# Kernel optimization log

Hardware: AMD Instinct MI355X
Metric: run time of the kernel (lower is better)

Reference implementation:

```python
import jax, jax.numpy as jnp
import numpy as np

B, S, T, D, ST, C = 128, 37, 2048, 256, 8, 2  # batch, sensors, time, d_model, static, classes
MERGED = D + ST


def setup_inputs() -> dict:
    key = jax.random.key(0)
    ks = jax.random.split(key, 14)
    u = lambda k, shape, fan: jax.random.uniform(k, shape, jnp.float32, -1.0, 1.0) / np.sqrt(fan)
    return {
        "x": jax.random.normal(ks[0], (B, S, T), jnp.float32),
        "static": jax.random.normal(ks[1], (B, ST), jnp.float32),
        "time": jax.random.uniform(ks[2], (B, T), jnp.float32),
        "sensor_mask": jax.random.randint(ks[3], (B, S, T), 0, 2).astype(jnp.int32),
        # learned params (torch Linear stored here as [in, out])
        "W_sensor": u(ks[4], (2 * S, D), 2 * S),
        "b_sensor": u(ks[5], (D,), 2 * S),
        "W_time": u(ks[6], (1, D), 1),
        "b_time": u(ks[7], (D,), 1),
        "W_static": u(ks[8], (ST, ST), ST),
        "b_static": u(ks[9], (ST,), ST),
        "W_merge": u(ks[10], (MERGED, MERGED), MERGED),
        "b_merge": u(ks[11], (MERGED,), MERGED),
        "W_cls": u(ks[12], (MERGED, C), MERGED),
        "b_cls": u(ks[13], (C,), MERGED),
    }


def reference(x, static, time, sensor_mask, W_sensor, b_sensor, W_time, b_time,
              W_static, b_static, W_merge, b_merge, W_cls, b_cls):
    # [B,S,T] -> [B,T,S]; concat measurements with (float) sensor mask -> [B,T,2S]
    x_t = jnp.transpose(x, (0, 2, 1))
    m_t = jnp.transpose(sensor_mask, (0, 2, 1)).astype(jnp.float32)
    x_time = jnp.concatenate([x_t, m_t], axis=2)
    # timestep valid-mask: any nonzero feature at that step
    mask = (jnp.sum(x_time != 0, axis=2) > 0).astype(jnp.float32)  # [B,T]
    # sensor embedding + time encoding
    h = jnp.einsum('btf,fd->btd', x_time, W_sensor) + b_sensor
    h = h + time[..., None] * W_time[0] + b_time  # Linear(1, D) on time
    # NOTE: Mamba2ForCausalLM(vocab_size=0) produces logits with size(-1)==0,
    # so the original forward falls back to last_hidden_states = x_time (= h).
    # masked mean pooling over time
    denom = jnp.clip(jnp.sum(mask, axis=1), 1e-9)[:, None]  # [B,1]
    pooled = jnp.sum(h * mask[..., None], axis=1) / denom  # [B,D]
    static_e = static @ W_static + b_static  # [B,ST]
    comb = jnp.concatenate([pooled, static_e], axis=1)  # [B,MERGED]
    comb = jax.nn.relu(comb @ W_merge + b_merge)
    return comb @ W_cls + b_cls  # [B,C]
```

## Files before the change

### kernel.cpp

```cpp
#include <hip/hip_runtime.h>
#include <hip/hip_bf16.h>

#define BB   128
#define SS   37
#define TT   2048
#define DD   256
#define STT  8
#define CC   2
#define MER  264
#define FF   74

#define NC    8
#define CHUNK (TT / NC)
#define RW    76
#define NSW   10

__global__ __launch_bounds__(256) void reduce_kernel(
    const float* __restrict__ x,
    const int*   __restrict__ smk,
    const float* __restrict__ tarr,
    float* __restrict__ red)
{
    const int blk   = blockIdx.x;
    const int b     = blk >> 3;
    const int chunk = blk & 7;
    const int t0    = chunk * CHUNK;
    const int wave  = threadIdx.x >> 6;
    const int lane  = threadIdx.x & 63;

    float ax[NSW];
    float am[NSW];
    unsigned nz = 0;

#pragma unroll
    for (int si = 0; si < NSW; ++si) {
        const int s = wave + 4 * si;
        if (s < SS) {
            const size_t base = ((size_t)(b * SS + s)) * TT + t0 + 4 * lane;
            const float4 xv = *(const float4*)(x + base);
            const int4   mv = *(const int4*)(smk + base);
            ax[si] = (xv.x + xv.y) + (xv.z + xv.w);
            am[si] = (float)((mv.x + mv.y) + (mv.z + mv.w));
            nz |= ((xv.x != 0.f) | (mv.x != 0)) ? 1u : 0u;
            nz |= ((xv.y != 0.f) | (mv.y != 0)) ? 2u : 0u;
            nz |= ((xv.z != 0.f) | (mv.z != 0)) ? 4u : 0u;
            nz |= ((xv.w != 0.f) | (mv.w != 0)) ? 8u : 0u;
        } else {
            ax[si] = 0.f; am[si] = 0.f;
        }
    }

    __shared__ unsigned nzp[4][64];
    nzp[wave][lane] = nz;
    __syncthreads();

    if (wave == 0) {
        const unsigned m = nzp[0][lane] | nzp[1][lane] | nzp[2][lane] | nzp[3][lane];
        const float4 tv = *(const float4*)(tarr + (size_t)b * TT + t0 + 4 * lane);
        float cnt = 0.f, tsum = 0.f;
        if (m & 1u) { cnt += 1.f; tsum += tv.x; }
        if (m & 2u) { cnt += 1.f; tsum += tv.y; }
        if (m & 4u) { cnt += 1.f; tsum += tv.z; }
        if (m & 8u) { cnt += 1.f; tsum += tv.w; }
        for (int off = 32; off; off >>= 1) {
            cnt  += __shfl_down(cnt,  off, 64);
            tsum += __shfl_down(tsum, off, 64);
        }
        if (lane == 0) {
            atomicAdd(&red[b * RW + 74], cnt);
            atomicAdd(&red[b * RW + 75], tsum);
        }
    }

#pragma unroll
    for (int si = 0; si < NSW; ++si) {
        const int s = wave + 4 * si;
        if (s < SS) {
            float vx = ax[si], vm = am[si];
            for (int off = 32; off; off >>= 1) {
                vx += __shfl_down(vx, off, 64);
                vm += __shfl_down(vm, off, 64);
            }
            if (lane == 0) {
                atomicAdd(&red[b * RW + s],      vx);
                atomicAdd(&red[b * RW + SS + s], vm);
            }
        }
    }
}

__global__ __launch_bounds__(320) void head_kernel(
    const float* __restrict__ red,
    const float* __restrict__ statics,
    const float* __restrict__ W_sensor,
    const float* __restrict__ b_sensor,
    const float* __restrict__ W_time,
    const float* __restrict__ b_time,
    const float* __restrict__ W_static,
    const float* __restrict__ b_static,
    const float* __restrict__ W_merge,
    const float* __restrict__ b_merge,
    const float* __restrict__ W_cls,
    const float* __restrict__ b_cls,
    float* __restrict__ out)
{
    const int b   = blockIdx.x;
    const int tid = threadIdx.x;

    __shared__ float sred[RW];
    __shared__ float comb[MER];
    __shared__ float comb2[MER];
    __shared__ float rbuf[10];

    if (tid < RW) sred[tid] = red[b * RW + tid];
    __syncthreads();

    const float smask = sred[74];
    const float stime = sred[75];
    const float inv   = 1.0f / fmaxf(smask, 1e-9f);

    if (tid < DD) {
        const int d = tid;
        float a0 = smask * (b_sensor[d] + b_time[d]) + stime * W_time[d];
        float a1 = 0.f;
#pragma unroll
        for (int f = 0; f < FF; f += 2) {
            a0 += sred[f]     * W_sensor[f * DD + d];
            a1 += sred[f + 1] * W_sensor[(f + 1) * DD + d];
        }
        comb[d] = (a0 + a1) * inv;
    } else if (tid < DD + STT) {
        const int j = tid - DD;
        float acc = b_static[j];
#pragma unroll
        for (int i = 0; i < STT; ++i)
            acc += statics[b * STT + i] * W_static[i * STT + j];
        comb[DD + j] = acc;
    }
    __syncthreads();

    if (tid < MER) {
        const int j = tid;
        float a[8];
#pragma unroll
        for (int k = 0; k < 8; ++k) a[k] = 0.f;
        for (int i = 0; i < MER; i += 8) {
#pragma unroll
            for (int k = 0; k < 8; ++k)
                a[k] += comb[i + k] * W_merge[(i + k) * MER + j];
        }
        const float acc = b_merge[j] +
            ((a[0] + a[1]) + (a[2] + a[3])) + ((a[4] + a[5]) + (a[6] + a[7]));
        comb2[j] = fmaxf(acc, 0.f);
    }
    __syncthreads();

    float c0 = 0.f, c1 = 0.f;
    if (tid < MER) {
        const float v = comb2[tid];
        c0 = v * W_cls[tid * CC];
        c1 = v * W_cls[tid * CC + 1];
    }
    for (int off = 32; off; off >>= 1) {
        c0 += __shfl_down(c0, off, 64);
        c1 += __shfl_down(c1, off, 64);
    }
    const int wv = tid >> 6, ln = tid & 63;
    if (ln == 0) { rbuf[wv] = c0; rbuf[5 + wv] = c1; }
    __syncthreads();
    if (tid == 0)
        out[b * CC + 0] = b_cls[0] + rbuf[0] + rbuf[1] + rbuf[2] + rbuf[3] + rbuf[4];
    if (tid == 1)
        out[b * CC + 1] = b_cls[1] + rbuf[5] + rbuf[6] + rbuf[7] + rbuf[8] + rbuf[9];
}

extern "C" void kernel_launch(void* const* d_in, const int* in_sizes, int n_in,
                              void* d_out, int out_size, void* d_ws, size_t ws_size,
                              hipStream_t stream) {
    const float* x        = (const float*)d_in[0];
    const float* statics  = (const float*)d_in[1];
    const float* tarr     = (const float*)d_in[2];
    const int*   smk      = (const int*)  d_in[3];
    const float* W_sensor = (const float*)d_in[4];
    const float* b_sensor = (const float*)d_in[5];
    const float* W_time   = (const float*)d_in[6];
    const float* b_time   = (const float*)d_in[7];
    const float* W_static = (const float*)d_in[8];
    const float* b_static = (const float*)d_in[9];
    const float* W_merge  = (const float*)d_in[10];
    const float* b_merge  = (const float*)d_in[11];
    const float* W_cls    = (const float*)d_in[12];
    const float* b_cls    = (const float*)d_in[13];
    float* out = (float*)d_out;
    float* red = (float*)d_ws;

    hipMemsetAsync(red, 0, (size_t)BB * RW * sizeof(float), stream);

    reduce_kernel<<<BB * NC, 256, 0, stream>>>(x, smk, tarr, red);
    head_kernel<<<BB, 320, 0, stream>>>(red, statics, W_sensor, b_sensor,
                                        W_time, b_time, W_static, b_static,
                                        W_merge, b_merge, W_cls, b_cls, out);
}
```

Baseline: 145.7 us.

## Replace atomics with per-block partial rows and drop memset

Halves the number of reduce blocks so each block covers two 256-step slices of time, accumulating both in registers. Each block now writes its partial sums to its own workspace row with plain stores instead of global atomicAdd. The head kernel then sums the four partial rows itself, which removes the hipMemsetAsync launch and the atomic contention. The trade-off is fewer blocks (512) with more loads in flight per thread, which may lower occupancy-driven latency hiding on a bandwidth-bound kernel.

```diff
diff --git a/kernel.cpp b/kernel.cpp
--- a/kernel.cpp
+++ b/kernel.cpp
@@ -10,8 +10,9 @@
 #define MER  264
 #define FF   74
 
-#define NC    8
+#define NC    4
 #define CHUNK (TT / NC)
+#define NJ    (CHUNK / 256)
 #define RW    76
 #define NSW   10
 
@@ -22,8 +23,8 @@
     float* __restrict__ red)
 {
     const int blk   = blockIdx.x;
-    const int b     = blk >> 3;
-    const int chunk = blk & 7;
+    const int b     = blk >> 2;
+    const int chunk = blk & 3;
     const int t0    = chunk * CHUNK;
     const int wave  = threadIdx.x >> 6;
     const int lane  = threadIdx.x & 63;
@@ -31,22 +32,27 @@
     float ax[NSW];
     float am[NSW];
     unsigned nz = 0;
-
-#pragma unroll
-    for (int si = 0; si < NSW; ++si) {
-        const int s = wave + 4 * si;
-        if (s < SS) {
-            const size_t base = ((size_t)(b * SS + s)) * TT + t0 + 4 * lane;
-            const float4 xv = *(const float4*)(x + base);
-            const int4   mv = *(const int4*)(smk + base);
-            ax[si] = (xv.x + xv.y) + (xv.z + xv.w);
-            am[si] = (float)((mv.x + mv.y) + (mv.z + mv.w));
-            nz |= ((xv.x != 0.f) | (mv.x != 0)) ? 1u : 0u;
-            nz |= ((xv.y != 0.f) | (mv.y != 0)) ? 2u : 0u;
-            nz |= ((xv.z != 0.f) | (mv.z != 0)) ? 4u : 0u;
-            nz |= ((xv.w != 0.f) | (mv.w != 0)) ? 8u : 0u;
-        } else {
-            ax[si] = 0.f; am[si] = 0.f;
+#pragma unroll
+    for (int i = 0; i < NSW; ++i) { ax[i] = 0.f; am[i] = 0.f; }
+
+#pragma unroll
+    for (int j = 0; j < NJ; ++j) {
+        const int tb = t0 + 256 * j + 4 * lane;
+#pragma unroll
+        for (int si = 0; si < NSW; ++si) {
+            const int s = wave + 4 * si;
+            if (s < SS) {
+                const size_t base = ((size_t)(b * SS + s)) * TT + tb;
+                const float4 xv = *(const float4*)(x + base);
+                const int4   mv = *(const int4*)(smk + base);
+                ax[si] += (xv.x + xv.y) + (xv.z + xv.w);
+                am[si] += (float)((mv.x + mv.y) + (mv.z + mv.w));
+                unsigned f = (unsigned)((xv.x != 0.f) | (mv.x != 0))
+                           | ((unsigned)((xv.y != 0.f) | (mv.y != 0)) << 1)
+                           | ((unsigned)((xv.z != 0.f) | (mv.z != 0)) << 2)
+                           | ((unsigned)((xv.w != 0.f) | (mv.w != 0)) << 3);
+                nz |= f << (4 * j);
+            }
         }
     }
 
@@ -54,22 +60,25 @@
     nzp[wave][lane] = nz;
     __syncthreads();
 
+    float* __restrict__ rrow = red + (size_t)blk * RW;
+
     if (wave == 0) {
         const unsigned m = nzp[0][lane] | nzp[1][lane] | nzp[2][lane] | nzp[3][lane];
-        const float4 tv = *(const float4*)(tarr + (size_t)b * TT + t0 + 4 * lane);
         float cnt = 0.f, tsum = 0.f;
-        if (m & 1u) { cnt += 1.f; tsum += tv.x; }
-        if (m & 2u) { cnt += 1.f; tsum += tv.y; }
-        if (m & 4u) { cnt += 1.f; tsum += tv.z; }
-        if (m & 8u) { cnt += 1.f; tsum += tv.w; }
+#pragma unroll
+        for (int j = 0; j < NJ; ++j) {
+            const float4 tv = *(const float4*)(tarr + (size_t)b * TT + t0 + 256 * j + 4 * lane);
+            const unsigned mj = (m >> (4 * j)) & 0xFu;
+            if (mj & 1u) { cnt += 1.f; tsum += tv.x; }
+            if (mj & 2u) { cnt += 1.f; tsum += tv.y; }
+            if (mj & 4u) { cnt += 1.f; tsum += tv.z; }
+            if (mj & 8u) { cnt += 1.f; tsum += tv.w; }
+        }
         for (int off = 32; off; off >>= 1) {
             cnt  += __shfl_down(cnt,  off, 64);
             tsum += __shfl_down(tsum, off, 64);
         }
-        if (lane == 0) {
-            atomicAdd(&red[b * RW + 74], cnt);
-            atomicAdd(&red[b * RW + 75], tsum);
-        }
+        if (lane == 0) { rrow[74] = cnt; rrow[75] = tsum; }
     }
 
 #pragma unroll
@@ -81,10 +90,7 @@
                 vx += __shfl_down(vx, off, 64);
                 vm += __shfl_down(vm, off, 64);
             }
-            if (lane == 0) {
-                atomicAdd(&red[b * RW + s],      vx);
-                atomicAdd(&red[b * RW + SS + s], vm);
-            }
+            if (lane == 0) { rrow[s] = vx; rrow[SS + s] = vm; }
         }
     }
 }
@@ -112,7 +118,10 @@
     __shared__ float comb2[MER];
     __shared__ float rbuf[10];
 
-    if (tid < RW) sred[tid] = red[b * RW + tid];
+    if (tid < RW) {
+        const float* rb = red + (size_t)b * NC * RW + tid;
+        sred[tid] = (rb[0] + rb[RW]) + (rb[2 * RW] + rb[3 * RW]);
+    }
     __syncthreads();
 
     const float smask = sred[74];
@@ -194,8 +203,6 @@
     float* out = (float*)d_out;
     float* red = (float*)d_ws;
 
-    hipMemsetAsync(red, 0, (size_t)BB * RW * sizeof(float), stream);
-
     reduce_kernel<<<BB * NC, 256, 0, stream>>>(x, smk, tarr, red);
     head_kernel<<<BB, 320, 0, stream>>>(red, statics, W_sensor, b_sensor,
                                         W_time, b_time, W_static, b_static,
```

Result: no change. 145.0 us (-0.5%).
